# Kernel tuning notes

Measured on AMD Instinct MI355X. Metric: run time of the kernel, lower is better.

## Reference

```python
import jax, jax.numpy as jnp
import numpy as np

B, I, H, O, E, K = 1024, 512, 2048, 512, 8, 2


def setup_inputs() -> dict:
    key = jax.random.key(0)
    k = jax.random.split(key, 7)
    s = 0.02
    return {
        "x": jax.random.normal(k[0], (B, I), dtype=jnp.float32),
        "Wg": jax.random.normal(k[1], (I, E), dtype=jnp.float32) * s,
        "bg": jnp.zeros((E,), dtype=jnp.float32),
        "W1": jax.random.normal(k[2], (E, I, H), dtype=jnp.float32) * s,
        "b1": jnp.zeros((E, H), dtype=jnp.float32),
        "W2": jax.random.normal(k[3], (E, H, O), dtype=jnp.float32) * s,
        "b2": jnp.zeros((E, O), dtype=jnp.float32),
    }


def reference(x, Wg, bg, W1, b1, W2, b2):
    # Gating: linear -> softmax -> top-k -> renormalize (inference path,
    # no dynamic expert creation / sleep bookkeeping).
    logits = x @ Wg + bg                      # [B, E]
    probs = jax.nn.softmax(logits, axis=-1)
    top_w, top_i = jax.lax.top_k(probs, K)    # [B, K]
    top_w = top_w / jnp.sum(top_w, axis=-1, keepdims=True)
    # Dense combine weights: zero for unselected experts -> identical math to
    # the per-expert mask-gather / weighted scatter-add in the torch loop.
    combine = jnp.zeros((x.shape[0], W1.shape[0]), dtype=x.dtype)
    combine = combine.at[jnp.arange(x.shape[0])[:, None], top_i].add(top_w)  # [B, E]
    # Expert MLPs (Linear -> ReLU -> Linear), batched over experts.
    h = jax.nn.relu(jnp.einsum("bi,eih->beh", x, W1) + b1[None])  # [B, E, H]
    y = jnp.einsum("beh,eho->beo", h, W2) + b2[None]              # [B, E, O]
    out = jnp.einsum("be,beo->bo", combine, y)                    # [B, O]
    return out
```

## Files before the change

kernel.cpp:

```cpp
#include <hip/hip_runtime.h>
#include <math.h>


#define B_TOK 1024
#define I_DIM 512
#define H_DIM 2048
#define O_DIM 512
#define E_NUM 8
#define CAP   1024

#define WS_COUNTS   0
#define WS_TOK_E    64
#define WS_TOK_W    8256
#define WS_TOK_SLOT 16448
#define WS_XB       65536
#define WS_HB       1114112
#define WS_Y4       34668544

typedef __attribute__((ext_vector_type(8))) __bf16 bf16x8;
typedef __attribute__((ext_vector_type(4))) __bf16 bf16x4;
typedef __attribute__((ext_vector_type(2))) __bf16 bf16x2;
typedef __attribute__((ext_vector_type(4))) float f32x4;

#define MFMA16 __builtin_amdgcn_mfma_f32_16x16x32_bf16
#define BSTR 520

__global__ __launch_bounds__(256) void gating_kernel(
    const float* __restrict__ x, const float* __restrict__ Wg,
    const float* __restrict__ bg, __bf16* __restrict__ xb,
    int* __restrict__ tok_e, float* __restrict__ tok_w)
{
    const int lane = threadIdx.x & 63;
    const int t = blockIdx.x * 4 + (threadIdx.x >> 6);
    const float4* x4 = (const float4*)(x + (size_t)t * I_DIM);
    float4 va = x4[lane], vb = x4[lane + 64];
    bf16x4 oa, ob;
    oa[0] = (__bf16)va.x; oa[1] = (__bf16)va.y;
    oa[2] = (__bf16)va.z; oa[3] = (__bf16)va.w;
    ob[0] = (__bf16)vb.x; ob[1] = (__bf16)vb.y;
    ob[2] = (__bf16)vb.z; ob[3] = (__bf16)vb.w;
    *(bf16x4*)(xb + (size_t)t * I_DIM + lane * 4) = oa;
    *(bf16x4*)(xb + (size_t)t * I_DIM + 256 + lane * 4) = ob;

    float acc[8];
#pragma unroll
    for (int e = 0; e < 8; ++e) acc[e] = 0.f;
    float xv[8] = {va.x, va.y, va.z, va.w, vb.x, vb.y, vb.z, vb.w};
#pragma unroll
    for (int u = 0; u < 8; ++u) {
        int i = (u < 4) ? (lane * 4 + u) : (256 + lane * 4 + u - 4);
        const float4* wr = (const float4*)(Wg + (size_t)i * 8);
        float4 wa = wr[0], wb2 = wr[1];
        acc[0] = fmaf(xv[u], wa.x, acc[0]);
        acc[1] = fmaf(xv[u], wa.y, acc[1]);
        acc[2] = fmaf(xv[u], wa.z, acc[2]);
        acc[3] = fmaf(xv[u], wa.w, acc[3]);
        acc[4] = fmaf(xv[u], wb2.x, acc[4]);
        acc[5] = fmaf(xv[u], wb2.y, acc[5]);
        acc[6] = fmaf(xv[u], wb2.z, acc[6]);
        acc[7] = fmaf(xv[u], wb2.w, acc[7]);
    }
#pragma unroll
    for (int off = 32; off > 0; off >>= 1)
#pragma unroll
        for (int e = 0; e < 8; ++e)
            acc[e] += __shfl_xor(acc[e], off, 64);
    if (lane == 0) {
        float l[8];
#pragma unroll
        for (int e = 0; e < 8; ++e) l[e] = acc[e] + bg[e];
        int e0 = 0;
        for (int e = 1; e < 8; ++e) if (l[e] > l[e0]) e0 = e;
        int e1 = (e0 == 0) ? 1 : 0;
        for (int e = 0; e < 8; ++e) {
            if (e == e0) continue;
            if (l[e] > l[e1]) e1 = e;
        }
        float w0 = 1.f / (1.f + expf(l[e1] - l[e0]));
        tok_e[t * 2]     = e0;
        tok_e[t * 2 + 1] = e1;
        tok_w[t * 2]     = w0;
        tok_w[t * 2 + 1] = 1.f - w0;
    }
}

template <bool IS_FC1>
__global__ __launch_bounds__(512, 4) void moe_gemm(
    const __bf16* __restrict__ A, const float* __restrict__ Wf,
    const float* __restrict__ bias,
    int* __restrict__ counts, const int* __restrict__ tok_e,
    int* __restrict__ tok_slot,
    __bf16* __restrict__ hb, float* __restrict__ y4)
{
    constexpr int NW   = IS_FC1 ? H_DIM : O_DIM;
    constexpr int ASTR = IS_FC1 ? I_DIM : H_DIM;

    const int bid = blockIdx.x;
    const int e = bid & 7;
    const int r = bid >> 3;
    const int nx = IS_FC1 ? r : (r & 15);
    const int kc = IS_FC1 ? 0 : (r >> 4);
    const int n0 = nx * 32;
    const int kb = kc * 512;
    const int off = e * CAP;
    const float* W = Wf + (size_t)e * (IS_FC1 ? I_DIM * H_DIM : H_DIM * O_DIM);

    __shared__ __align__(16) __bf16 Bs[32 * BSTR];
    __shared__ int sl[IS_FC1 ? CAP : 1];
    __shared__ int sMe;

    const int tid = threadIdx.x;
    const int lane = tid & 63, w = tid >> 6;
    const int l15 = lane & 15, q = lane >> 4;

#pragma unroll
    for (int i = 0; i < 4; ++i) {
        const int u = tid + 512 * i;
        const int p = u >> 3, c4 = u & 7;
        const float* wp = W + (size_t)(kb + 2 * p) * NW + n0 + c4 * 4;
        float4 r0 = *(const float4*)wp;
        float4 r1 = *(const float4*)(wp + NW);
        const float* f0 = (const float*)&r0;
        const float* f1 = (const float*)&r1;
#pragma unroll
        for (int j = 0; j < 4; ++j) {
            bf16x2 pk;
            pk[0] = (__bf16)f0[j];
            pk[1] = (__bf16)f1[j];
            *(bf16x2*)&Bs[(size_t)(c4 * 4 + j) * BSTR + 2 * p] = pk;
        }
    }

    if (IS_FC1 && w == 0) {
        int cnt = 0;
#pragma unroll
        for (int bb = 0; bb < 2; ++bb) {
            int vals[16];
#pragma unroll
            for (int c = 0; c < 16; ++c)
                vals[c] = tok_e[(bb * 16 + c) * 64 + lane];
#pragma unroll
            for (int c = 0; c < 16; ++c) {
                const int gidx = (bb * 16 + c) * 64 + lane;
                const bool hit = (vals[c] == e);
                const unsigned long long mk = __ballot(hit);
                if (hit) {
                    const int pos = cnt + __popcll(mk & ((1ull << lane) - 1));
                    sl[pos] = gidx >> 1;
                    if (nx == 0) tok_slot[gidx] = off + pos;
                }
                cnt += __popcll(mk);
            }
        }
        if (lane == 0) {
            sMe = cnt;
            if (nx == 0) counts[e] = cnt;
        }
    }
    __syncthreads();
    const int Me = IS_FC1 ? sMe : counts[e];

    for (int m0 = w * 32; m0 < Me; m0 += 256) {
        int mA = m0 + l15;      if (mA >= Me) mA = Me - 1;
        int mB = m0 + 16 + l15; if (mB >= Me) mB = Me - 1;
        const __bf16 *a0, *a1;
        if (IS_FC1) {
            a0 = A + (size_t)sl[mA] * ASTR + q * 8;
            a1 = A + (size_t)sl[mB] * ASTR + q * 8;
        } else {
            a0 = A + (size_t)(off + mA) * ASTR + kb + q * 8;
            a1 = A + (size_t)(off + mB) * ASTR + kb + q * 8;
        }

        f32x4 acc[2][2] = {};
#pragma unroll 4
        for (int ks = 0; ks < 16; ++ks) {
            bf16x8 af0 = *(const bf16x8*)(a0 + ks * 32);
            bf16x8 af1 = *(const bf16x8*)(a1 + ks * 32);
#pragma unroll
            for (int jj = 0; jj < 2; ++jj) {
                bf16x8 bf = *(const bf16x8*)
                    &Bs[(size_t)(jj * 16 + l15) * BSTR + ks * 32 + q * 8];
                acc[0][jj] = MFMA16(af0, bf, acc[0][jj], 0, 0, 0);
                acc[1][jj] = MFMA16(af1, bf, acc[1][jj], 0, 0, 0);
            }
        }
#pragma unroll
        for (int jj = 0; jj < 2; ++jj) {
            const int gn = n0 + jj * 16 + l15;
            if (IS_FC1) {
                const float bv = bias[e * H_DIM + gn];
#pragma unroll
                for (int i = 0; i < 2; ++i)
#pragma unroll
                    for (int rr = 0; rr < 4; ++rr) {
                        int m = m0 + i * 16 + q * 4 + rr;
                        if (m < Me) {
                            float v = acc[i][jj][rr] + bv;
                            hb[(size_t)(off + m) * H_DIM + gn] =
                                (__bf16)fmaxf(v, 0.f);
                        }
                    }
            } else {
#pragma unroll
                for (int i = 0; i < 2; ++i)
#pragma unroll
                    for (int rr = 0; rr < 4; ++rr) {
                        int m = m0 + i * 16 + q * 4 + rr;
                        if (m < Me)
                            y4[((size_t)kc * (E_NUM * CAP) + off + m) * O_DIM + gn] =
                                acc[i][jj][rr];
                    }
            }
        }
    }
}

__global__ __launch_bounds__(256) void combine_kernel(
    const float* __restrict__ y4, const float* __restrict__ b2,
    const int* __restrict__ tok_slot, const int* __restrict__ tok_e,
    const float* __restrict__ tok_w, float* __restrict__ out)
{
    const int idx = blockIdx.x * 256 + threadIdx.x;
    const int t = idx >> 7;
    const int c = (idx & 127) * 4;
    float4 sum = {0.f, 0.f, 0.f, 0.f};
#pragma unroll
    for (int k = 0; k < 2; ++k) {
        const int s = tok_slot[t * 2 + k];
        const int e = tok_e[t * 2 + k];
        const float wgt = tok_w[t * 2 + k];
        float4 a = *(const float4*)(b2 + (size_t)e * O_DIM + c);
#pragma unroll
        for (int kc = 0; kc < 4; ++kc) {
            float4 v = *(const float4*)
                (y4 + ((size_t)kc * (E_NUM * CAP) + s) * O_DIM + c);
            a.x += v.x; a.y += v.y; a.z += v.z; a.w += v.w;
        }
        sum.x += wgt * a.x; sum.y += wgt * a.y;
        sum.z += wgt * a.z; sum.w += wgt * a.w;
    }
    *(float4*)(out + (size_t)t * O_DIM + c) = sum;
}

extern "C" void kernel_launch(void* const* d_in, const int* in_sizes, int n_in,
                              void* d_out, int out_size, void* d_ws, size_t ws_size,
                              hipStream_t stream)
{
    const float* x  = (const float*)d_in[0];
    const float* Wg = (const float*)d_in[1];
    const float* bg = (const float*)d_in[2];
    const float* W1 = (const float*)d_in[3];
    const float* b1 = (const float*)d_in[4];
    const float* W2 = (const float*)d_in[5];
    const float* b2 = (const float*)d_in[6];
    float* out = (float*)d_out;
    char* ws = (char*)d_ws;

    int*    counts   = (int*)(ws + WS_COUNTS);
    int*    tok_e    = (int*)(ws + WS_TOK_E);
    float*  tok_w    = (float*)(ws + WS_TOK_W);
    int*    tok_slot = (int*)(ws + WS_TOK_SLOT);
    __bf16* xb       = (__bf16*)(ws + WS_XB);
    __bf16* hb       = (__bf16*)(ws + WS_HB);
    float*  y4       = (float*)(ws + WS_Y4);

    gating_kernel<<<B_TOK / 4, 256, 0, stream>>>(x, Wg, bg, xb, tok_e, tok_w);
    moe_gemm<true><<<512, 512, 0, stream>>>(
        xb, W1, b1, counts, tok_e, tok_slot, hb, y4);
    moe_gemm<false><<<512, 512, 0, stream>>>(
        hb, W2, b2, counts, tok_e, tok_slot, hb, y4);
    combine_kernel<<<(B_TOK * O_DIM / 4) / 256, 256, 0, stream>>>(
        y4, b2, tok_slot, tok_e, tok_w, out);
}
```

Before: 154.9 us.

## Double-buffer A and B tiles in LDS with async global-to-LDS loads

Rewrites the expert GEMM so that A rows are streamed into LDS with global_load_lds and weight chunks are converted to bf16 into LDS. Both use double buffering over 64-wide K chunks, and the tile becomes 128x64 split across a 4x2 wave grid. FC2 drops its K-split from 4 to 2 and launches half as many blocks, which halves the partial-output traffic read by the combine kernel. In exchange there is a barrier per K chunk, weights are reloaded for every M tile, and each block has less parallel work.

Measured after the change: 156.0 us. No clear change (+0.7%).

```diff
diff --git a/kernel.cpp b/kernel.cpp
--- a/kernel.cpp
+++ b/kernel.cpp
@@ -15,7 +15,7 @@
 #define WS_TOK_SLOT 16448
 #define WS_XB       65536
 #define WS_HB       1114112
-#define WS_Y4       34668544
+#define WS_Y2       34668544
 
 typedef __attribute__((ext_vector_type(8))) __bf16 bf16x8;
 typedef __attribute__((ext_vector_type(4))) __bf16 bf16x4;
@@ -23,7 +23,15 @@
 typedef __attribute__((ext_vector_type(4))) float f32x4;
 
 #define MFMA16 __builtin_amdgcn_mfma_f32_16x16x32_bf16
-#define BSTR 520
+#define BSTRB 72
+
+__device__ __forceinline__ void gll16(const __bf16* g, __bf16* l)
+{
+    __builtin_amdgcn_global_load_lds(
+        (const __attribute__((address_space(1))) uint32_t*)g,
+        (__attribute__((address_space(3))) uint32_t*)(uintptr_t)(void*)l,
+        16, 0, 0);
+}
 
 __global__ __launch_bounds__(256) void gating_kernel(
     const float* __restrict__ x, const float* __restrict__ Wg,
@@ -90,46 +98,32 @@
     const float* __restrict__ bias,
     int* __restrict__ counts, const int* __restrict__ tok_e,
     int* __restrict__ tok_slot,
-    __bf16* __restrict__ hb, float* __restrict__ y4)
+    __bf16* __restrict__ hb, float* __restrict__ y2)
 {
     constexpr int NW   = IS_FC1 ? H_DIM : O_DIM;
     constexpr int ASTR = IS_FC1 ? I_DIM : H_DIM;
-
-    const int bid = blockIdx.x;
-    const int e = bid & 7;
-    const int r = bid >> 3;
-    const int nx = IS_FC1 ? r : (r & 15);
-    const int kc = IS_FC1 ? 0 : (r >> 4);
-    const int n0 = nx * 32;
-    const int kb = kc * 512;
-    const int off = e * CAP;
+    constexpr int NCH  = IS_FC1 ? 8 : 16;
+
+    const int bid  = blockIdx.x;
+    const int e    = bid & 7;
+    const int rest = bid >> 3;
+    const int nx   = IS_FC1 ? (rest & 31) : (rest & 7);
+    const int my   = IS_FC1 ? (rest >> 5) : ((rest >> 3) & 1);
+    const int kc   = IS_FC1 ? 0 : (rest >> 4);
+    const int n0   = nx * 64;
+    const int k0   = kc * 1024;
+    const int off  = e * CAP;
     const float* W = Wf + (size_t)e * (IS_FC1 ? I_DIM * H_DIM : H_DIM * O_DIM);
 
-    __shared__ __align__(16) __bf16 Bs[32 * BSTR];
+    __shared__ __align__(16) __bf16 As[2][16 * 512];
+    __shared__ __align__(16) __bf16 Bsh[2][64 * BSTRB];
     __shared__ int sl[IS_FC1 ? CAP : 1];
     __shared__ int sMe;
 
     const int tid = threadIdx.x;
     const int lane = tid & 63, w = tid >> 6;
     const int l15 = lane & 15, q = lane >> 4;
-
-#pragma unroll
-    for (int i = 0; i < 4; ++i) {
-        const int u = tid + 512 * i;
-        const int p = u >> 3, c4 = u & 7;
-        const float* wp = W + (size_t)(kb + 2 * p) * NW + n0 + c4 * 4;
-        float4 r0 = *(const float4*)wp;
-        float4 r1 = *(const float4*)(wp + NW);
-        const float* f0 = (const float*)&r0;
-        const float* f1 = (const float*)&r1;
-#pragma unroll
-        for (int j = 0; j < 4; ++j) {
-            bf16x2 pk;
-            pk[0] = (__bf16)f0[j];
-            pk[1] = (__bf16)f1[j];
-            *(bf16x2*)&Bs[(size_t)(c4 * 4 + j) * BSTR + 2 * p] = pk;
-        }
-    }
+    const int wm = w >> 1, wn = w & 1;
 
     if (IS_FC1 && w == 0) {
         int cnt = 0;
@@ -147,56 +141,98 @@
                 if (hit) {
                     const int pos = cnt + __popcll(mk & ((1ull << lane) - 1));
                     sl[pos] = gidx >> 1;
-                    if (nx == 0) tok_slot[gidx] = off + pos;
+                    if (nx == 0 && my == 0) tok_slot[gidx] = off + pos;
                 }
                 cnt += __popcll(mk);
             }
         }
         if (lane == 0) {
             sMe = cnt;
-            if (nx == 0) counts[e] = cnt;
+            if (nx == 0 && my == 0) counts[e] = cnt;
         }
     }
     __syncthreads();
     const int Me = IS_FC1 ? sMe : counts[e];
-
-    for (int m0 = w * 32; m0 < Me; m0 += 256) {
-        int mA = m0 + l15;      if (mA >= Me) mA = Me - 1;
-        int mB = m0 + 16 + l15; if (mB >= Me) mB = Me - 1;
-        const __bf16 *a0, *a1;
-        if (IS_FC1) {
-            a0 = A + (size_t)sl[mA] * ASTR + q * 8;
-            a1 = A + (size_t)sl[mB] * ASTR + q * 8;
-        } else {
-            a0 = A + (size_t)(off + mA) * ASTR + kb + q * 8;
-            a1 = A + (size_t)(off + mB) * ASTR + kb + q * 8;
-        }
+    if (Me == 0) return;
+
+    const int p = tid >> 4, c4 = tid & 15;
+    const float* wB = W + (size_t)(k0 + 2 * p) * NW + n0 + c4 * 4;
+
+    for (int mb = my * 128; mb < Me; mb += 256) {
+        int rA = mb + w * 16 + l15; if (rA >= Me) rA = Me - 1;
+        const __bf16* gA = IS_FC1 ? (A + (size_t)sl[rA] * ASTR)
+                                  : (A + (size_t)(off + rA) * ASTR + k0);
+
+        gll16(gA + q * 8,      &As[0][(2 * w) * 512]);
+        gll16(gA + 32 + q * 8, &As[0][(2 * w + 1) * 512]);
+        {
+            float4 r0 = *(const float4*)wB;
+            float4 r1 = *(const float4*)(wB + NW);
+            const float* f0 = (const float*)&r0;
+            const float* f1 = (const float*)&r1;
+#pragma unroll
+            for (int j = 0; j < 4; ++j) {
+                bf16x2 pk;
+                pk[0] = (__bf16)f0[j];
+                pk[1] = (__bf16)f1[j];
+                *(bf16x2*)&Bsh[0][(c4 * 4 + j) * BSTRB + 2 * p] = pk;
+            }
+        }
+        __syncthreads();
 
         f32x4 acc[2][2] = {};
-#pragma unroll 4
-        for (int ks = 0; ks < 16; ++ks) {
-            bf16x8 af0 = *(const bf16x8*)(a0 + ks * 32);
-            bf16x8 af1 = *(const bf16x8*)(a1 + ks * 32);
-#pragma unroll
-            for (int jj = 0; jj < 2; ++jj) {
-                bf16x8 bf = *(const bf16x8*)
-                    &Bs[(size_t)(jj * 16 + l15) * BSTR + ks * 32 + q * 8];
-                acc[0][jj] = MFMA16(af0, bf, acc[0][jj], 0, 0, 0);
-                acc[1][jj] = MFMA16(af1, bf, acc[1][jj], 0, 0, 0);
-            }
-        }
-#pragma unroll
-        for (int jj = 0; jj < 2; ++jj) {
-            const int gn = n0 + jj * 16 + l15;
+        for (int c = 0; c < NCH; ++c) {
+            const int cb = c & 1, nb = cb ^ 1;
+            const bool more = (c + 1 < NCH);
+            float4 r0, r1;
+            if (more) {
+                const float* wp = wB + (size_t)(c + 1) * 64 * NW;
+                r0 = *(const float4*)wp;
+                r1 = *(const float4*)(wp + NW);
+                gll16(gA + (c + 1) * 64 + q * 8,      &As[nb][(2 * w) * 512]);
+                gll16(gA + (c + 1) * 64 + 32 + q * 8, &As[nb][(2 * w + 1) * 512]);
+            }
+#pragma unroll
+            for (int sk = 0; sk < 2; ++sk) {
+                bf16x8 a0 = *(const bf16x8*)
+                    &As[cb][((wm * 2 + 0) * 2 + sk) * 512 + lane * 8];
+                bf16x8 a1 = *(const bf16x8*)
+                    &As[cb][((wm * 2 + 1) * 2 + sk) * 512 + lane * 8];
+                bf16x8 b0 = *(const bf16x8*)
+                    &Bsh[cb][((wn * 2 + 0) * 16 + l15) * BSTRB + sk * 32 + q * 8];
+                bf16x8 b1 = *(const bf16x8*)
+                    &Bsh[cb][((wn * 2 + 1) * 16 + l15) * BSTRB + sk * 32 + q * 8];
+                acc[0][0] = MFMA16(a0, b0, acc[0][0], 0, 0, 0);
+                acc[0][1] = MFMA16(a0, b1, acc[0][1], 0, 0, 0);
+                acc[1][0] = MFMA16(a1, b0, acc[1][0], 0, 0, 0);
+                acc[1][1] = MFMA16(a1, b1, acc[1][1], 0, 0, 0);
+            }
+            if (more) {
+                const float* f0 = (const float*)&r0;
+                const float* f1 = (const float*)&r1;
+#pragma unroll
+                for (int j = 0; j < 4; ++j) {
+                    bf16x2 pk;
+                    pk[0] = (__bf16)f0[j];
+                    pk[1] = (__bf16)f1[j];
+                    *(bf16x2*)&Bsh[nb][(c4 * 4 + j) * BSTRB + 2 * p] = pk;
+                }
+            }
+            __syncthreads();
+        }
+
+#pragma unroll
+        for (int j = 0; j < 2; ++j) {
+            const int gn = n0 + (wn * 2 + j) * 16 + l15;
             if (IS_FC1) {
                 const float bv = bias[e * H_DIM + gn];
 #pragma unroll
                 for (int i = 0; i < 2; ++i)
 #pragma unroll
                     for (int rr = 0; rr < 4; ++rr) {
-                        int m = m0 + i * 16 + q * 4 + rr;
+                        int m = mb + (wm * 2 + i) * 16 + q * 4 + rr;
                         if (m < Me) {
-                            float v = acc[i][jj][rr] + bv;
+                            float v = acc[i][j][rr] + bv;
                             hb[(size_t)(off + m) * H_DIM + gn] =
                                 (__bf16)fmaxf(v, 0.f);
                         }
@@ -206,10 +242,10 @@
                 for (int i = 0; i < 2; ++i)
 #pragma unroll
                     for (int rr = 0; rr < 4; ++rr) {
-                        int m = m0 + i * 16 + q * 4 + rr;
+                        int m = mb + (wm * 2 + i) * 16 + q * 4 + rr;
                         if (m < Me)
-                            y4[((size_t)kc * (E_NUM * CAP) + off + m) * O_DIM + gn] =
-                                acc[i][jj][rr];
+                            y2[((size_t)kc * (E_NUM * CAP) + off + m) * O_DIM + gn] =
+                                acc[i][j][rr];
                     }
             }
         }
@@ -217,7 +253,7 @@
 }
 
 __global__ __launch_bounds__(256) void combine_kernel(
-    const float* __restrict__ y4, const float* __restrict__ b2,
+    const float* __restrict__ y2, const float* __restrict__ b2,
     const int* __restrict__ tok_slot, const int* __restrict__ tok_e,
     const float* __restrict__ tok_w, float* __restrict__ out)
 {
@@ -232,9 +268,9 @@
         const float wgt = tok_w[t * 2 + k];
         float4 a = *(const float4*)(b2 + (size_t)e * O_DIM + c);
 #pragma unroll
-        for (int kc = 0; kc < 4; ++kc) {
+        for (int kc = 0; kc < 2; ++kc) {
             float4 v = *(const float4*)
-                (y4 + ((size_t)kc * (E_NUM * CAP) + s) * O_DIM + c);
+                (y2 + ((size_t)kc * (E_NUM * CAP) + s) * O_DIM + c);
             a.x += v.x; a.y += v.y; a.z += v.z; a.w += v.w;
         }
         sum.x += wgt * a.x; sum.y += wgt * a.y;
@@ -263,13 +299,13 @@
     int*    tok_slot = (int*)(ws + WS_TOK_SLOT);
     __bf16* xb       = (__bf16*)(ws + WS_XB);
     __bf16* hb       = (__bf16*)(ws + WS_HB);
-    float*  y4       = (float*)(ws + WS_Y4);
+    float*  y2       = (float*)(ws + WS_Y2);
 
     gating_kernel<<<B_TOK / 4, 256, 0, stream>>>(x, Wg, bg, xb, tok_e, tok_w);
     moe_gemm<true><<<512, 512, 0, stream>>>(
-        xb, W1, b1, counts, tok_e, tok_slot, hb, y4);
-    moe_gemm<false><<<512, 512, 0, stream>>>(
-        hb, W2, b2, counts, tok_e, tok_slot, hb, y4);
+        xb, W1, b1, counts, tok_e, tok_slot, hb, y2);
+    moe_gemm<false><<<256, 512, 0, stream>>>(
+        hb, W2, b2, counts, tok_e, tok_slot, hb, y2);
     combine_kernel<<<(B_TOK * O_DIM / 4) / 256, 256, 0, stream>>>(
-        y4, b2, tok_slot, tok_e, tok_w, out);
-}
+        y2, b2, tok_slot, tok_e, tok_w, out);
+}
```
